# Performance work log

Measured on AMD Instinct MI355X. Metric: run time of the kernel, lower is better.

## Reference

```python
import jax, jax.numpy as jnp
import numpy as np

# dims
B, Nt, Ln, Lv = 16, 64, 256, 4      # batch, trees/batch, nodes/tree, value tokens/node
D = 256                              # embedding_dim
VOCAB, NTYPE = 32000, 64
M, Ls = 128, 4                       # story memory slots, tokens per slot
HOPS = 3                             # max_hops
COMP_STEP = 4                        # max tree depth = max(kb_n_layers)
LEVELS = [0, 1, 16, 64, 160, Ln]     # node index ranges per depth 0..4


def setup_inputs() -> dict:
    rng = np.random.default_rng(0)
    key = jax.random.key(0)
    ks = jax.random.split(key, 12)

    # --- tree structure: depth per node, father index in previous level ---
    depth = np.zeros(Ln, np.int64)
    father = np.zeros((B, Nt, Ln), np.int64)
    for lvl in range(1, 5):
        lo, hi = LEVELS[lvl], LEVELS[lvl + 1]
        depth[lo:hi] = lvl
        father[..., lo:hi] = rng.integers(LEVELS[lvl - 1], LEVELS[lvl], (B, Nt, hi - lo))
    father[..., 0] = Ln  # root's father = pad slot (torch -1 wraps to last index)
    kb_fathers = np.concatenate([father, np.full((B, Nt, 1), Ln, np.int64)], -1)  # [B,Nt,Ln+1]
    nl = np.broadcast_to(depth, (B, Nt, Ln))
    kb_n_layers = np.concatenate([nl, np.full((B, Nt, 1), -1, np.int64)], -1)     # [B,Nt,Ln+1]

    kb_values = rng.integers(1, VOCAB, (B, Nt, Ln, Lv))
    kb_types = rng.integers(1, NTYPE, (B, Nt, Ln))
    story = rng.integers(1, VOCAB, (B, M, Ls))
    decoder_input = rng.integers(1, VOCAB, (B,))

    s = 1.0 / np.sqrt(D)
    C = 0.1 * jax.random.normal(ks[0], (HOPS + 1, VOCAB, D), jnp.float32)
    C = C.at[:, 0].set(0.0)  # padding_idx = 0
    T_emb = 0.1 * jax.random.normal(ks[1], (NTYPE, D), jnp.float32)
    T_emb = T_emb.at[0].set(0.0)
    return {
        'decoder_input': jnp.asarray(decoder_input),
        'story': jnp.asarray(story),
        'hidden': 0.1 * jax.random.normal(ks[2], (1, B, D), jnp.float32),
        'kb_values': jnp.asarray(kb_values),
        'kb_types': jnp.asarray(kb_types),
        'kb_fathers': jnp.asarray(kb_fathers),
        'kb_n_layers': jnp.asarray(kb_n_layers),
        'C': C,
        'T_emb': T_emb,
        'Wq': s * jax.random.normal(ks[3], (D, D), jnp.float32),
        'Wk': s * jax.random.normal(ks[4], (D, D), jnp.float32),
        'Wv': s * jax.random.normal(ks[5], (D, D), jnp.float32),
        'W1_w': s * jax.random.normal(ks[6], (VOCAB, 2 * D), jnp.float32),
        'W1_b': jnp.zeros((VOCAB,), jnp.float32),
        'W_ih': s * jax.random.normal(ks[7], (3 * D, D), jnp.float32),
        'W_hh': s * jax.random.normal(ks[8], (3 * D, D), jnp.float32),
        'b_ih': jnp.zeros((3 * D,), jnp.float32),
        'b_hh': jnp.zeros((3 * D,), jnp.float32),
    }


def _forward(decoder_input, story, hidden, kb_values, kb_types, kb_fathers, kb_n_layers,
             C, T_emb, Wq, Wk, Wv, W1_w, W1_b, W_ih, W_hh, b_ih, b_hh):
    C0 = C[0]
    # ensemble: node embed = type_embed * sum(value token embeds)   [B,Nt,Ln,D]
    node = T_emb[kb_types] * C0[kb_values].sum(-2)
    node = jnp.concatenate([node, jnp.zeros((B, Nt, 1, D), node.dtype)], axis=2)  # pad slot
    nl = COMP_STEP - 1 - kb_n_layers  # adjusted layer counter
    base = jnp.arange(B * Nt).reshape(B, Nt, 1) * (Ln + 1)
    seg = (base + kb_fathers).reshape(-1)  # flat father ids for scatter-add

    def body(i, carry):
        node, nl = carry
        nxt = jax.ops.segment_sum(node.reshape(-1, D), seg,
                                  num_segments=B * Nt * (Ln + 1)).reshape(B, Nt, Ln + 1, D)
        node = node + nxt * (nl == 0)[..., None].astype(node.dtype)
        return (node, nl - 1)

    node, _ = jax.lax.fori_loop(0, COMP_STEP, body, (node, nl))
    roots = node[:, :, 0]                                   # [B,Nt,D]
    bias = jnp.where(roots.sum(-1) == 0, -1e9, 0.0)         # attention_bias [B,Nt]

    # compute_global_ranking: QKV attention over tree roots
    h = hidden[-1]                                          # [B,D]
    w = jax.nn.softmax(jnp.einsum('bnd,bd->bn', roots @ Wk.T, h @ Wq.T) + bias, axis=1)
    feat = jnp.einsum('bn,bnd->bd', w, roots @ Wv.T)        # kb_attn_features

    # single GRU step (PyTorch gate order r,z,n)
    x = C0[decoder_input]
    gi = x @ W_ih.T + b_ih
    gh = h @ W_hh.T + b_hh
    ir, iz, inn = jnp.split(gi, 3, -1)
    hr, hz, hn = jnp.split(gh, 3, -1)
    r = jax.nn.sigmoid(ir + hr)
    z = jax.nn.sigmoid(iz + hz)
    n = jnp.tanh(inn + r * hn)
    h_new = (1.0 - z) * n + z * h
    u = h_new + feat                                        # cur_state

    # ptrMemDecoder (Mem2Seq-style hops over story memory)
    p_vocab = None
    logits = None
    for hop in range(HOPS):
        m_A = C[hop][story].sum(2)                          # [B,M,D]
        logits = jnp.einsum('bmd,bd->bm', m_A, u)
        prob = jax.nn.softmax(logits, axis=1)
        m_C = C[hop + 1][story].sum(2)
        o = jnp.einsum('bm,bmd->bd', prob, m_C)
        if hop == 0:
            p_vocab = jnp.concatenate([u, o], -1) @ W1_w.T + W1_b
        u = u + o
    p_ptr = logits
    return p_ptr, p_vocab, h_new


def reference(decoder_input, story, hidden, kb_values, kb_types, kb_fathers, kb_n_layers,
              C, T_emb, Wq, Wk, Wv, W1_w, W1_b, W_ih, W_hh, b_ih, b_hh):
    return _forward(decoder_input, story, hidden, kb_values, kb_types, kb_fathers, kb_n_layers,
                    C, T_emb, Wq, Wk, Wv, W1_w, W1_b, W_ih, W_hh, b_ih, b_hh)
```

## Files before the change

kernel.cpp:

```cpp
#include <hip/hip_runtime.h>
#include <hip/hip_bf16.h>
#include <math.h>

#define B_ 16
#define NT 64
#define LN 256
#define LV 4
#define D_ 256
#define VOCAB_ 32000
#define M_ 128
#define LS 4
#define ECAP 352

typedef unsigned short ushort_t;
typedef unsigned int uint_t;

__device__ __forceinline__ ushort_t f2bf(float f) {
  uint_t u = __float_as_uint(f);
  uint_t r = u + 0x7FFFu + ((u >> 16) & 1u);
  return (ushort_t)(r >> 16);
}
__device__ __forceinline__ float bflo(uint_t u) {
  return __uint_as_float(u << 16);
}
__device__ __forceinline__ float bfhi(uint_t u) {
  return __uint_as_float(u & 0xFFFF0000u);
}

#define NB_S (3 * B_ * M_)
#define NB_CONV 2048
#define NB_TR 192
#define NB_TQK 256
#define NB_WVT 64
#define NB_BKT (B_ * NT)
__global__ __launch_bounds__(256) void k_prep(
    const int* __restrict__ story, const float* __restrict__ C,
    const float* __restrict__ W_ih, const float* __restrict__ W_hh,
    const float* __restrict__ Wq, const float* __restrict__ Wk,
    const float* __restrict__ Wv, const int* __restrict__ kb_values,
    const int* __restrict__ kb_types, float* __restrict__ S,
    ushort_t* __restrict__ C0h, float* __restrict__ W_ihT,
    float* __restrict__ W_hhT, float* __restrict__ TQK,
    float* __restrict__ WvT, int* __restrict__ entries,
    int* __restrict__ counts) {
  __shared__ __align__(16) char praw[6400];
  float* smem = (float*)praw;
  int blk = blockIdx.x, tid = threadIdx.x;
  if (blk < NB_S) {
    int h = blk / (B_ * M_);
    int bm = blk % (B_ * M_);
    const int* st = story + (size_t)bm * LS;
    const float* Ch = C + (size_t)h * VOCAB_ * D_;
    float s = Ch[(size_t)st[0] * D_ + tid] + Ch[(size_t)st[1] * D_ + tid] +
              Ch[(size_t)st[2] * D_ + tid] + Ch[(size_t)st[3] * D_ + tid];
    S[(size_t)blk * D_ + tid] = s;
  } else if (blk < NB_S + NB_CONV) {
    int n4 = VOCAB_ * D_ / 4;
    for (int i = (blk - NB_S) * 256 + tid; i < n4; i += NB_CONV * 256) {
      float4 f = ((const float4*)C)[i];
      uint2 packed;
      packed.x = (uint_t)f2bf(f.x) | ((uint_t)f2bf(f.y) << 16);
      packed.y = (uint_t)f2bf(f.z) | ((uint_t)f2bf(f.w) << 16);
      ((uint2*)C0h)[i] = packed;
    }
  } else if (blk < NB_S + NB_CONV + 2 * NB_TR) {
    int t = blk - (NB_S + NB_CONV);
    const float* W = W_ih;
    float* WT = W_ihT;
    if (t >= NB_TR) { t -= NB_TR; W = W_hh; WT = W_hhT; }
    const int R = 768;
    int tr = t % (R / 32), tc = t / (R / 32);
    int tx = tid & 31, ty = tid >> 5;
#pragma unroll
    for (int k = 0; k < 4; ++k)
      smem[(ty + 8 * k) * 33 + tx] =
          W[(size_t)(tr * 32 + ty + 8 * k) * D_ + tc * 32 + tx];
    __syncthreads();
#pragma unroll
    for (int k = 0; k < 4; ++k)
      WT[(size_t)(tc * 32 + ty + 8 * k) * R + tr * 32 + tx] =
          smem[tx * 33 + ty + 8 * k];
  } else if (blk < NB_S + NB_CONV + 2 * NB_TR + NB_TQK) {
    int j = blk - (NB_S + NB_CONV + 2 * NB_TR);
    smem[tid] = Wq[(size_t)tid * D_ + j];
    __syncthreads();
    float acc = 0.f;
#pragma unroll 8
    for (int k = 0; k < D_; ++k) acc += smem[k] * Wk[(size_t)k * D_ + tid];
    TQK[(size_t)j * D_ + tid] = acc;
  } else if (blk < NB_S + NB_CONV + 2 * NB_TR + NB_TQK + NB_WVT) {
    int t = blk - (NB_S + NB_CONV + 2 * NB_TR + NB_TQK);
    int tr = t & 7, tc = t >> 3;
    int tx = tid & 31, ty = tid >> 5;
#pragma unroll
    for (int k = 0; k < 4; ++k)
      smem[(ty + 8 * k) * 33 + tx] =
          Wv[(size_t)(tr * 32 + ty + 8 * k) * D_ + tc * 32 + tx];
    __syncthreads();
#pragma unroll
    for (int k = 0; k < 4; ++k)
      WvT[(size_t)(tc * 32 + ty + 8 * k) * D_ + tr * 32 + tx] =
          smem[tx * 33 + ty + 8 * k];
  } else {
    int bn = blk - (NB_S + NB_CONV + 2 * NB_TR + NB_TQK + NB_WVT);
    int* sval = (int*)praw;
    int* stype = sval + 1024;
    int* sbin = stype + 256;
    int* srng = sbin + 256;
    const int* vp = kb_values + (size_t)bn * LN * LV;
    for (int i = tid; i < LN * LV; i += 256) sval[i] = vp[i];
    stype[tid] = kb_types[(size_t)bn * LN + tid];
    sbin[tid] = 0;
    __syncthreads();
    int ty = stype[tid];
    int vv[4];
#pragma unroll
    for (int j = 0; j < 4; ++j) {
      vv[j] = sval[tid * 4 + j];
      atomicAdd(&sbin[((vv[j] >> 13) << 6) | ty], 1);
    }
    __syncthreads();
    if (tid < 64) {
      int run = 0;
#pragma unroll
      for (int c = 0; c < 4; ++c) {
        int x = sbin[c * 64 + tid];
        int orig = x;
        for (int o = 1; o < 64; o <<= 1) {
          int y = __shfl_up(x, o);
          if ((int)tid >= o) x += y;
        }
        sbin[c * 64 + tid] = x - orig + run;
        run += __shfl(x, 63);
      }
    }
    __syncthreads();
    if (tid < 4) {
      srng[tid] = sbin[tid << 6];
      int e = (tid == 3) ? (LN * LV) : sbin[(tid + 1) << 6];
      counts[bn * 4 + tid] = min(e - sbin[tid << 6], ECAP);
    }
    __syncthreads();
#pragma unroll
    for (int j = 0; j < 4; ++j) {
      int v = vv[j];
      int r = v >> 13;
      int pos = atomicAdd(&sbin[(r << 6) | ty], 1) - srng[r];
      if (pos < ECAP)
        entries[(size_t)(bn * 4 + r) * ECAP + pos] = v | (ty << 16);
    }
  }
}

#define NBG 4096
__global__ __launch_bounds__(256) void k_rootsg(
    const int* __restrict__ counts, const int* __restrict__ entries,
    const ushort_t* __restrict__ C0h, const float* __restrict__ T_emb,
    const int* __restrict__ dec, const float* __restrict__ C0,
    const float* __restrict__ hidden, const float* __restrict__ W_ihT,
    const float* __restrict__ W_hhT, const float* __restrict__ TQK,
    const float* __restrict__ b_ih, const float* __restrict__ b_hh,
    float* __restrict__ part, float* __restrict__ gi, float* __restrict__ gh,
    float* __restrict__ tvec) {
  __shared__ __align__(16) char smem_raw[6144];
  int blk = blockIdx.x, tid = threadIdx.x;
  if (blk < NBG) {
    int slot = blk & 7;
    int r = slot >> 1;
    int bn = ((blk >> 3) << 1) | (slot & 1);
    int bucket = bn * 4 + r;
    int cnt = counts[bucket];
    const int* ge = entries + (size_t)bucket * ECAP;
    int* ent = (int*)smem_raw;
    float* psum = (float*)(smem_raw + 1536);
    for (int i = tid; i < cnt; i += 256) ent[i] = ge[i];
    __syncthreads();
    int lane = tid & 63, team = tid >> 6;
    int chunk = ((cnt + 15) >> 4) << 2;
    int k0 = team * chunk;
    int k1 = min(cnt, k0 + chunk);
    float a0 = 0.f, a1 = 0.f, a2 = 0.f, a3 = 0.f;
    int k = k0;
#pragma unroll 2
    for (; k + 4 <= k1; k += 4) {
      int4 e4 = *(const int4*)(ent + k);
      const uint2* r0 = (const uint2*)(C0h + ((size_t)(e4.x & 0xFFFF) << 8));
      const uint2* r1 = (const uint2*)(C0h + ((size_t)(e4.y & 0xFFFF) << 8));
      const uint2* r2 = (const uint2*)(C0h + ((size_t)(e4.z & 0xFFFF) << 8));
      const uint2* r3 = (const uint2*)(C0h + ((size_t)(e4.w & 0xFFFF) << 8));
      uint2 u0 = r0[lane];
      uint2 u1 = r1[lane];
      uint2 u2 = r2[lane];
      uint2 u3 = r3[lane];
      float4 t0 = ((const float4*)(T_emb + ((size_t)(e4.x >> 16) << 8)))[lane];
      float4 t1 = ((const float4*)(T_emb + ((size_t)(e4.y >> 16) << 8)))[lane];
      float4 t2 = ((const float4*)(T_emb + ((size_t)(e4.z >> 16) << 8)))[lane];
      float4 t3 = ((const float4*)(T_emb + ((size_t)(e4.w >> 16) << 8)))[lane];
      a0 += t0.x * bflo(u0.x) + t1.x * bflo(u1.x) + t2.x * bflo(u2.x) +
            t3.x * bflo(u3.x);
      a1 += t0.y * bfhi(u0.x) + t1.y * bfhi(u1.x) + t2.y * bfhi(u2.x) +
            t3.y * bfhi(u3.x);
      a2 += t0.z * bflo(u0.y) + t1.z * bflo(u1.y) + t2.z * bflo(u2.y) +
            t3.z * bflo(u3.y);
      a3 += t0.w * bfhi(u0.y) + t1.w * bfhi(u1.y) + t2.w * bfhi(u2.y) +
            t3.w * bfhi(u3.y);
    }
    for (; k < k1; ++k) {
      int e = ent[k];
      uint2 u = ((const uint2*)(C0h + ((size_t)(e & 0xFFFF) << 8)))[lane];
      float4 t = ((const float4*)(T_emb + ((size_t)(e >> 16) << 8)))[lane];
      a0 += t.x * bflo(u.x);
      a1 += t.y * bfhi(u.x);
      a2 += t.z * bflo(u.y);
      a3 += t.w * bfhi(u.y);
    }
    psum[team * D_ + 4 * lane + 0] = a0;
    psum[team * D_ + 4 * lane + 1] = a1;
    psum[team * D_ + 4 * lane + 2] = a2;
    psum[team * D_ + 4 * lane + 3] = a3;
    __syncthreads();
    float rsl = psum[0 * D_ + tid] + psum[1 * D_ + tid] + psum[2 * D_ + tid] +
                psum[3 * D_ + tid];
    part[(size_t)bucket * D_ + tid] = rsl;
  } else {
    int g = blk - NBG;
    float* xs = (float*)smem_raw;
    float acc[B_];
    if (g < 3) {
      int i = g * 256 + tid;
      float bias = b_ih[i];
#pragma unroll
      for (int b = 0; b < B_; ++b) acc[b] = bias;
      for (int c = 0; c < 4; ++c) {
        __syncthreads();
#pragma unroll
        for (int idx = tid; idx < B_ * 64; idx += 256) {
          int b = idx >> 6, jj = idx & 63;
          xs[idx] = C0[(size_t)dec[b] * D_ + c * 64 + jj];
        }
        __syncthreads();
#pragma unroll 4
        for (int jj = 0; jj < 64; ++jj) {
          float w = W_ihT[(size_t)(c * 64 + jj) * 768 + i];
#pragma unroll
          for (int b = 0; b < B_; ++b) acc[b] += xs[b * 64 + jj] * w;
        }
      }
#pragma unroll
      for (int b = 0; b < B_; ++b) gi[(size_t)b * 768 + i] = acc[b];
    } else if (g < 6) {
      int i = (g - 3) * 256 + tid;
      float bias = b_hh[i];
#pragma unroll
      for (int b = 0; b < B_; ++b) acc[b] = bias;
      for (int c = 0; c < 4; ++c) {
        __syncthreads();
#pragma unroll
        for (int idx = tid; idx < B_ * 64; idx += 256) {
          int b = idx >> 6, jj = idx & 63;
          xs[idx] = hidden[b * D_ + c * 64 + jj];
        }
        __syncthreads();
#pragma unroll 4
        for (int jj = 0; jj < 64; ++jj) {
          float w = W_hhT[(size_t)(c * 64 + jj) * 768 + i];
#pragma unroll
          for (int b = 0; b < B_; ++b) acc[b] += xs[b * 64 + jj] * w;
        }
      }
#pragma unroll
      for (int b = 0; b < B_; ++b) gh[(size_t)b * 768 + i] = acc[b];
    } else {
#pragma unroll
      for (int b = 0; b < B_; ++b) acc[b] = 0.f;
      for (int c = 0; c < 4; ++c) {
        __syncthreads();
#pragma unroll
        for (int idx = tid; idx < B_ * 64; idx += 256) {
          int b = idx >> 6, jj = idx & 63;
          xs[idx] = hidden[b * D_ + c * 64 + jj];
        }
        __syncthreads();
#pragma unroll 4
        for (int jj = 0; jj < 64; ++jj) {
          float w = TQK[(size_t)(c * 64 + jj) * D_ + tid];
#pragma unroll
          for (int b = 0; b < B_; ++b) acc[b] += xs[b * 64 + jj] * w;
        }
      }
#pragma unroll
      for (int b = 0; b < B_; ++b) tvec[b * D_ + tid] = acc[b];
    }
  }
}

__global__ __launch_bounds__(256) void k_mid(
    const float* __restrict__ part, const float* __restrict__ tvec,
    const float* __restrict__ S, float* __restrict__ scores,
    float* __restrict__ ST, float* __restrict__ rsum) {
  int blk = blockIdx.x, tid = threadIdx.x;
  if (blk < 1024) {
    int b = blk >> 6;
    const float* p = part + (size_t)blk * 4 * D_;
    float rv = p[tid] + p[D_ + tid] + p[2 * D_ + tid] + p[3 * D_ + tid];
    rsum[(size_t)blk * D_ + tid] = rv;
    float sc = rv * tvec[b * D_ + tid];
    float sm = rv;
    __shared__ float red[8];
    int lane = tid & 63, wave = tid >> 6;
    for (int o = 32; o > 0; o >>= 1) {
      sc += __shfl_xor(sc, o);
      sm += __shfl_xor(sm, o);
    }
    if (lane == 0) { red[wave] = sc; red[4 + wave] = sm; }
    __syncthreads();
    if (tid == 0) {
      float SC = red[0] + red[1] + red[2] + red[3];
      float SM = red[4] + red[5] + red[6] + red[7];
      scores[blk] = (SM == 0.0f) ? SC - 1000000000.0f : SC;
    }
  } else {
    int t = blk - 1024;
    int hb = t >> 5;
    int tile = t & 31;
    int tm = tile & 3, td = tile >> 2;
    int tx = tid & 31, ty = tid >> 5;
    __shared__ float sm2[32 * 33];
    const float* Sp = S + (size_t)hb * M_ * D_;
    float* STp = ST + (size_t)hb * D_ * M_;
#pragma unroll
    for (int k = 0; k < 4; ++k)
      sm2[(ty + 8 * k) * 33 + tx] =
          Sp[(size_t)(tm * 32 + ty + 8 * k) * D_ + td * 32 + tx];
    __syncthreads();
#pragma unroll
    for (int k = 0; k < 4; ++k)
      STp[(size_t)(td * 32 + ty + 8 * k) * M_ + tm * 32 + tx] =
          sm2[tx * 33 + ty + 8 * k];
  }
}

__global__ __launch_bounds__(256) void k_chain(
    const float* __restrict__ scores, const float* __restrict__ rsum,
    const float* __restrict__ WvT, const float* __restrict__ gi,
    const float* __restrict__ gh, const float* __restrict__ hidden,
    const float* __restrict__ S, const float* __restrict__ ST,
    float* __restrict__ h_new_out, float* __restrict__ cat,
    float* __restrict__ p_ptr) {
  int b = blockIdx.x, tid = threadIdx.x;
  __shared__ float wsh[NT], rs[D_], us[D_], lo[M_], loB[M_], pr[M_];
  if (tid < NT) {
    float s = scores[b * NT + tid];
    float m = s;
    for (int o = 32; o > 0; o >>= 1) m = fmaxf(m, __shfl_xor(m, o));
    float e = expf(s - m);
    float sum = e;
    for (int o = 32; o > 0; o >>= 1) sum += __shfl_xor(sum, o);
    wsh[tid] = e / sum;
  }
  __syncthreads();
  float rb = 0.f;
#pragma unroll 16
  for (int n = 0; n < NT; ++n)
    rb += wsh[n] * rsum[(size_t)(b * NT + n) * D_ + tid];
  rs[tid] = rb;
  __syncthreads();
  float feat = 0.f;
#pragma unroll 16
  for (int j = 0; j < D_; ++j) feat += rs[j] * WvT[(size_t)j * D_ + tid];
  {
    float i_r = gi[(size_t)b * 768 + tid];
    float i_z = gi[(size_t)b * 768 + 256 + tid];
    float i_n = gi[(size_t)b * 768 + 512 + tid];
    float h_r = gh[(size_t)b * 768 + tid];
    float h_z = gh[(size_t)b * 768 + 256 + tid];
    float h_n = gh[(size_t)b * 768 + 512 + tid];
    float h = hidden[b * D_ + tid];
    float r = 1.f / (1.f + expf(-(i_r + h_r)));
    float z = 1.f / (1.f + expf(-(i_z + h_z)));
    float nn = tanhf(i_n + r * h_n);
    float hn = (1.f - z) * nn + z * h;
    h_new_out[b * D_ + tid] = hn;
    float u0 = hn + feat;
    us[tid] = u0;
    cat[b * 512 + tid] = u0;
  }
  __syncthreads();
  for (int h = 0; h < 3; ++h) {
    {
      int m = tid & 127;
      int half = tid >> 7;
      const float* STp = ST + (((size_t)h * B_ + b) * D_ + half * 128) * M_;
      float l = 0.f;
#pragma unroll 16
      for (int d = 0; d < 128; ++d)
        l += us[half * 128 + d] * STp[(size_t)d * M_ + m];
      if (half == 0) lo[m] = l; else loB[m] = l;
    }
    __syncthreads();
    if (h == 2) {
      if (tid < M_) p_ptr[b * M_ + tid] = lo[tid] + loB[tid];
      break;
    }
    if (tid < 64) {
      float l0 = lo[tid] + loB[tid], l1 = lo[tid + 64] + loB[tid + 64];
      float a = fmaxf(l0, l1);
      for (int o = 32; o > 0; o >>= 1) a = fmaxf(a, __shfl_xor(a, o));
      float e0 = expf(l0 - a), e1 = expf(l1 - a);
      float s = e0 + e1;
      for (int o = 32; o > 0; o >>= 1) s += __shfl_xor(s, o);
      pr[tid] = e0 / s;
      pr[tid + 64] = e1 / s;
    }
    __syncthreads();
    {
      const float* Sn = S + (((size_t)(h + 1) * B_ + b) * M_) * D_;
      float o = 0.f;
#pragma unroll 16
      for (int m = 0; m < M_; ++m) o += pr[m] * Sn[(size_t)m * D_ + tid];
      if (h == 0) cat[b * 512 + D_ + tid] = o;
      us[tid] += o;
    }
    __syncthreads();
  }
}

__global__ __launch_bounds__(256) void k_pvocab(
    const float* __restrict__ cat, const float* __restrict__ W1_w,
    const float* __restrict__ W1_b, float* __restrict__ out) {
  int blk = blockIdx.x, tid = threadIdx.x;
  int row = tid & 63, q = tid >> 6;
  int v = blk * 64 + row;
  __shared__ float cs[B_ * 512];
  __shared__ float ps[3][64][B_];
  for (int i = tid; i < B_ * 512; i += 256) cs[i] = cat[i];
  __syncthreads();
  const float4* wrow = (const float4*)(W1_w + (size_t)v * 512 + q * 128);
  float acc[B_];
#pragma unroll
  for (int b = 0; b < B_; ++b) acc[b] = 0.f;
#pragma unroll 4
  for (int k4 = 0; k4 < 32; ++k4) {
    float4 w = wrow[k4];
#pragma unroll
    for (int b = 0; b < B_; ++b) {
      const float* c = &cs[b * 512 + q * 128 + k4 * 4];
      acc[b] += w.x * c[0] + w.y * c[1] + w.z * c[2] + w.w * c[3];
    }
  }
  if (q > 0) {
#pragma unroll
    for (int b = 0; b < B_; ++b) ps[q - 1][row][b] = acc[b];
  }
  __syncthreads();
  if (q == 0) {
    float bb = W1_b[v];
#pragma unroll
    for (int b = 0; b < B_; ++b)
      out[(size_t)b * VOCAB_ + v] =
          acc[b] + ps[0][row][b] + ps[1][row][b] + ps[2][row][b] + bb;
  }
}

extern "C" void kernel_launch(void* const* d_in, const int* in_sizes, int n_in,
                              void* d_out, int out_size, void* d_ws,
                              size_t ws_size, hipStream_t stream) {
  const int* decoder_input = (const int*)d_in[0];
  const int* story = (const int*)d_in[1];
  const float* hidden = (const float*)d_in[2];
  const int* kb_values = (const int*)d_in[3];
  const int* kb_types = (const int*)d_in[4];
  const float* C = (const float*)d_in[7];
  const float* T_emb = (const float*)d_in[8];
  const float* Wq = (const float*)d_in[9];
  const float* Wk = (const float*)d_in[10];
  const float* Wv = (const float*)d_in[11];
  const float* W1_w = (const float*)d_in[12];
  const float* W1_b = (const float*)d_in[13];
  const float* W_ih = (const float*)d_in[14];
  const float* W_hh = (const float*)d_in[15];
  const float* b_ih = (const float*)d_in[16];
  const float* b_hh = (const float*)d_in[17];

  float* out = (float*)d_out;
  float* p_ptr = out;
  float* p_vocab = out + B_ * M_;
  float* h_new = out + B_ * M_ + B_ * VOCAB_;

  float* ws = (float*)d_ws;
  float* S = ws;
  float* part = S + 3 * B_ * M_ * D_;
  float* rsum = part + B_ * NT * 4 * D_;
  float* cat = rsum + B_ * NT * D_;
  float* scores = cat + B_ * 512;
  float* gi = scores + B_ * NT;
  float* gh = gi + B_ * 768;
  float* tvec = gh + B_ * 768;
  int* counts = (int*)(tvec + B_ * D_);
  ushort_t* C0h = (ushort_t*)(counts + 4096);
  float* wtmp = (float*)(C0h + (size_t)VOCAB_ * D_);
  float* W_ihT = wtmp;
  float* W_hhT = W_ihT + 768 * D_;
  float* TQK = W_hhT + 768 * D_;
  int* entries = (int*)(TQK + D_ * D_);
  float* ST = wtmp;
  float* WvT = wtmp + (458752 + 1441792);

  hipLaunchKernelGGL(
      k_prep, dim3(NB_S + NB_CONV + 2 * NB_TR + NB_TQK + NB_WVT + NB_BKT),
      dim3(256), 0, stream, story, C, W_ih, W_hh, Wq, Wk, Wv, kb_values,
      kb_types, S, C0h, W_ihT, W_hhT, TQK, WvT, entries, counts);
  hipLaunchKernelGGL(k_rootsg, dim3(NBG + 7), dim3(256), 0, stream, counts,
                     entries, C0h, T_emb, decoder_input, C, hidden, W_ihT,
                     W_hhT, TQK, b_ih, b_hh, part, gi, gh, tvec);
  hipLaunchKernelGGL(k_mid, dim3(1024 + 1536), dim3(256), 0, stream, part,
                     tvec, S, scores, ST, rsum);
  hipLaunchKernelGGL(k_chain, dim3(B_), dim3(256), 0, stream, scores, rsum,
                     WvT, gi, gh, hidden, S, ST, h_new, cat, p_ptr);
  hipLaunchKernelGGL(k_pvocab, dim3(VOCAB_ / 64), dim3(256), 0, stream, cat,
                     W1_w, W1_b, p_vocab);
}
```

Baseline: 402.0 us.

## Stage T_emb in shared memory and assign one bucket per wave in k_rootsg

Restructures the gather kernel so that each 512-thread block first loads all 63 non-pad type-embedding rows into 63KB of LDS. Each wave then processes one whole bucket on its own and writes its float4 result directly, removing the per-block entry staging and the cross-team reduction. Entry indices are read straight from global memory and made wave-uniform with readfirstlane. The grid shrinks from 4096 to 512 gather blocks, and the GRU/TQK side blocks keep only half their threads busy. In exchange, every block pays a large LDS fill, occupancy drops because of the LDS size, and wave-level load imbalance becomes possible.

```diff
diff --git a/kernel.cpp b/kernel.cpp
--- a/kernel.cpp
+++ b/kernel.cpp
@@ -152,8 +152,8 @@
   }
 }
 
-#define NBG 4096
-__global__ __launch_bounds__(256) void k_rootsg(
+#define NBG 512
+__global__ __launch_bounds__(512) void k_rootsg(
     const int* __restrict__ counts, const int* __restrict__ entries,
     const ushort_t* __restrict__ C0h, const float* __restrict__ T_emb,
     const int* __restrict__ dec, const float* __restrict__ C0,
@@ -162,40 +162,38 @@
     const float* __restrict__ b_ih, const float* __restrict__ b_hh,
     float* __restrict__ part, float* __restrict__ gi, float* __restrict__ gh,
     float* __restrict__ tvec) {
-  __shared__ __align__(16) char smem_raw[6144];
+  __shared__ __align__(16) char smem_raw[64512];
   int blk = blockIdx.x, tid = threadIdx.x;
   if (blk < NBG) {
+    const float4* Tg = (const float4*)(T_emb + D_);
+    float4* t4s = (float4*)smem_raw;
+    for (int i = tid; i < 63 * 64; i += 512) t4s[i] = Tg[i];
+    __syncthreads();
+    int wid = tid >> 6, lane = tid & 63;
     int slot = blk & 7;
-    int r = slot >> 1;
-    int bn = ((blk >> 3) << 1) | (slot & 1);
+    int r = slot >> 1, sub = slot & 1;
+    int bn = (((blk >> 3) << 1) | sub) * 8 + wid;
     int bucket = bn * 4 + r;
     int cnt = counts[bucket];
     const int* ge = entries + (size_t)bucket * ECAP;
-    int* ent = (int*)smem_raw;
-    float* psum = (float*)(smem_raw + 1536);
-    for (int i = tid; i < cnt; i += 256) ent[i] = ge[i];
-    __syncthreads();
-    int lane = tid & 63, team = tid >> 6;
-    int chunk = ((cnt + 15) >> 4) << 2;
-    int k0 = team * chunk;
-    int k1 = min(cnt, k0 + chunk);
+    const int4* ge4 = (const int4*)ge;
     float a0 = 0.f, a1 = 0.f, a2 = 0.f, a3 = 0.f;
-    int k = k0;
+    int k = 0;
 #pragma unroll 2
-    for (; k + 4 <= k1; k += 4) {
-      int4 e4 = *(const int4*)(ent + k);
-      const uint2* r0 = (const uint2*)(C0h + ((size_t)(e4.x & 0xFFFF) << 8));
-      const uint2* r1 = (const uint2*)(C0h + ((size_t)(e4.y & 0xFFFF) << 8));
-      const uint2* r2 = (const uint2*)(C0h + ((size_t)(e4.z & 0xFFFF) << 8));
-      const uint2* r3 = (const uint2*)(C0h + ((size_t)(e4.w & 0xFFFF) << 8));
-      uint2 u0 = r0[lane];
-      uint2 u1 = r1[lane];
-      uint2 u2 = r2[lane];
-      uint2 u3 = r3[lane];
-      float4 t0 = ((const float4*)(T_emb + ((size_t)(e4.x >> 16) << 8)))[lane];
-      float4 t1 = ((const float4*)(T_emb + ((size_t)(e4.y >> 16) << 8)))[lane];
-      float4 t2 = ((const float4*)(T_emb + ((size_t)(e4.z >> 16) << 8)))[lane];
-      float4 t3 = ((const float4*)(T_emb + ((size_t)(e4.w >> 16) << 8)))[lane];
+    for (; k + 4 <= cnt; k += 4) {
+      int4 e4 = ge4[k >> 2];
+      int ex = __builtin_amdgcn_readfirstlane(e4.x);
+      int ey = __builtin_amdgcn_readfirstlane(e4.y);
+      int ez = __builtin_amdgcn_readfirstlane(e4.z);
+      int ew = __builtin_amdgcn_readfirstlane(e4.w);
+      uint2 u0 = ((const uint2*)(C0h + ((size_t)(ex & 0xFFFF) << 8)))[lane];
+      uint2 u1 = ((const uint2*)(C0h + ((size_t)(ey & 0xFFFF) << 8)))[lane];
+      uint2 u2 = ((const uint2*)(C0h + ((size_t)(ez & 0xFFFF) << 8)))[lane];
+      uint2 u3 = ((const uint2*)(C0h + ((size_t)(ew & 0xFFFF) << 8)))[lane];
+      float4 t0 = t4s[((ex >> 16) - 1) * 64 + lane];
+      float4 t1 = t4s[((ey >> 16) - 1) * 64 + lane];
+      float4 t2 = t4s[((ez >> 16) - 1) * 64 + lane];
+      float4 t3 = t4s[((ew >> 16) - 1) * 64 + lane];
       a0 += t0.x * bflo(u0.x) + t1.x * bflo(u1.x) + t2.x * bflo(u2.x) +
             t3.x * bflo(u3.x);
       a1 += t0.y * bfhi(u0.x) + t1.y * bfhi(u1.x) + t2.y * bfhi(u2.x) +
@@ -205,91 +203,94 @@
       a3 += t0.w * bfhi(u0.y) + t1.w * bfhi(u1.y) + t2.w * bfhi(u2.y) +
             t3.w * bfhi(u3.y);
     }
-    for (; k < k1; ++k) {
-      int e = ent[k];
+    for (; k < cnt; ++k) {
+      int e = __builtin_amdgcn_readfirstlane(ge[k]);
       uint2 u = ((const uint2*)(C0h + ((size_t)(e & 0xFFFF) << 8)))[lane];
-      float4 t = ((const float4*)(T_emb + ((size_t)(e >> 16) << 8)))[lane];
+      float4 t = t4s[((e >> 16) - 1) * 64 + lane];
       a0 += t.x * bflo(u.x);
       a1 += t.y * bfhi(u.x);
       a2 += t.z * bflo(u.y);
       a3 += t.w * bfhi(u.y);
     }
-    psum[team * D_ + 4 * lane + 0] = a0;
-    psum[team * D_ + 4 * lane + 1] = a1;
-    psum[team * D_ + 4 * lane + 2] = a2;
-    psum[team * D_ + 4 * lane + 3] = a3;
-    __syncthreads();
-    float rsl = psum[0 * D_ + tid] + psum[1 * D_ + tid] + psum[2 * D_ + tid] +
-                psum[3 * D_ + tid];
-    part[(size_t)bucket * D_ + tid] = rsl;
+    float4 res;
+    res.x = a0; res.y = a1; res.z = a2; res.w = a3;
+    ((float4*)(part + (size_t)bucket * D_))[lane] = res;
   } else {
     int g = blk - NBG;
     float* xs = (float*)smem_raw;
     float acc[B_];
+    int i = (g < 3 ? g : g - 3) * 256 + tid;
     if (g < 3) {
-      int i = g * 256 + tid;
-      float bias = b_ih[i];
+      float bias = (tid < 256) ? b_ih[i] : 0.f;
 #pragma unroll
       for (int b = 0; b < B_; ++b) acc[b] = bias;
       for (int c = 0; c < 4; ++c) {
         __syncthreads();
-#pragma unroll
-        for (int idx = tid; idx < B_ * 64; idx += 256) {
+        for (int idx = tid; idx < B_ * 64; idx += 512) {
           int b = idx >> 6, jj = idx & 63;
           xs[idx] = C0[(size_t)dec[b] * D_ + c * 64 + jj];
         }
         __syncthreads();
+        if (tid < 256) {
 #pragma unroll 4
-        for (int jj = 0; jj < 64; ++jj) {
-          float w = W_ihT[(size_t)(c * 64 + jj) * 768 + i];
-#pragma unroll
-          for (int b = 0; b < B_; ++b) acc[b] += xs[b * 64 + jj] * w;
-        }
-      }
-#pragma unroll
-      for (int b = 0; b < B_; ++b) gi[(size_t)b * 768 + i] = acc[b];
+          for (int jj = 0; jj < 64; ++jj) {
+            float w = W_ihT[(size_t)(c * 64 + jj) * 768 + i];
+#pragma unroll
+            for (int b = 0; b < B_; ++b) acc[b] += xs[b * 64 + jj] * w;
+          }
+        }
+      }
+      if (tid < 256) {
+#pragma unroll
+        for (int b = 0; b < B_; ++b) gi[(size_t)b * 768 + i] = acc[b];
+      }
     } else if (g < 6) {
-      int i = (g - 3) * 256 + tid;
-      float bias = b_hh[i];
+      float bias = (tid < 256) ? b_hh[i] : 0.f;
 #pragma unroll
       for (int b = 0; b < B_; ++b) acc[b] = bias;
       for (int c = 0; c < 4; ++c) {
         __syncthreads();
-#pragma unroll
-        for (int idx = tid; idx < B_ * 64; idx += 256) {
+        for (int idx = tid; idx < B_ * 64; idx += 512) {
           int b = idx >> 6, jj = idx & 63;
           xs[idx] = hidden[b * D_ + c * 64 + jj];
         }
         __syncthreads();
+        if (tid < 256) {
 #pragma unroll 4
-        for (int jj = 0; jj < 64; ++jj) {
-          float w = W_hhT[(size_t)(c * 64 + jj) * 768 + i];
-#pragma unroll
-          for (int b = 0; b < B_; ++b) acc[b] += xs[b * 64 + jj] * w;
-        }
-      }
-#pragma unroll
-      for (int b = 0; b < B_; ++b) gh[(size_t)b * 768 + i] = acc[b];
+          for (int jj = 0; jj < 64; ++jj) {
+            float w = W_hhT[(size_t)(c * 64 + jj) * 768 + i];
+#pragma unroll
+            for (int b = 0; b < B_; ++b) acc[b] += xs[b * 64 + jj] * w;
+          }
+        }
+      }
+      if (tid < 256) {
+#pragma unroll
+        for (int b = 0; b < B_; ++b) gh[(size_t)b * 768 + i] = acc[b];
+      }
     } else {
 #pragma unroll
       for (int b = 0; b < B_; ++b) acc[b] = 0.f;
       for (int c = 0; c < 4; ++c) {
         __syncthreads();
-#pragma unroll
-        for (int idx = tid; idx < B_ * 64; idx += 256) {
+        for (int idx = tid; idx < B_ * 64; idx += 512) {
           int b = idx >> 6, jj = idx & 63;
           xs[idx] = hidden[b * D_ + c * 64 + jj];
         }
         __syncthreads();
+        if (tid < 256) {
 #pragma unroll 4
-        for (int jj = 0; jj < 64; ++jj) {
-          float w = TQK[(size_t)(c * 64 + jj) * D_ + tid];
-#pragma unroll
-          for (int b = 0; b < B_; ++b) acc[b] += xs[b * 64 + jj] * w;
-        }
-      }
-#pragma unroll
-      for (int b = 0; b < B_; ++b) tvec[b * D_ + tid] = acc[b];
+          for (int jj = 0; jj < 64; ++jj) {
+            float w = TQK[(size_t)(c * 64 + jj) * D_ + tid];
+#pragma unroll
+            for (int b = 0; b < B_; ++b) acc[b] += xs[b * 64 + jj] * w;
+          }
+        }
+      }
+      if (tid < 256) {
+#pragma unroll
+        for (int b = 0; b < B_; ++b) tvec[b * D_ + tid] = acc[b];
+      }
     }
   }
 }
@@ -510,7 +511,7 @@
       k_prep, dim3(NB_S + NB_CONV + 2 * NB_TR + NB_TQK + NB_WVT + NB_BKT),
       dim3(256), 0, stream, story, C, W_ih, W_hh, Wq, Wk, Wv, kb_values,
       kb_types, S, C0h, W_ihT, W_hhT, TQK, WvT, entries, counts);
-  hipLaunchKernelGGL(k_rootsg, dim3(NBG + 7), dim3(256), 0, stream, counts,
+  hipLaunchKernelGGL(k_rootsg, dim3(NBG + 7), dim3(512), 0, stream, counts,
                      entries, C0h, T_emb, decoder_input, C, hidden, W_ihT,
                      W_hhT, TQK, b_ih, b_hh, part, gi, gh, tvec);
   hipLaunchKernelGGL(k_mid, dim3(1024 + 1536), dim3(256), 0, stream, part,
```

New measurement: 389.9 us. 1.03x faster.
